# Optimization experiments

Hardware: AMD Instinct MI355X
Metric: run time of the kernel (lower is better)

The kernel has to match this reference:

```python
import jax, jax.numpy as jnp
import numpy as np

B, C, H, W = 8, 512, 64, 64
D = C // 8  # qk_downscale = 8


def setup_inputs() -> dict:
    key = jax.random.key(0)
    k1, k2, k3, k4, k5 = jax.random.split(key, 5)
    scale = 1.0 / np.sqrt(C)
    return {
        "x": jax.random.normal(k1, (B, C, H, W), dtype=jnp.float32),
        "Wq": jax.random.normal(k2, (D, C), dtype=jnp.float32) * scale,
        "Wk": jax.random.normal(k3, (D, C), dtype=jnp.float32) * scale,
        "Wv": jax.random.normal(k4, (C, C), dtype=jnp.float32) * scale,
        "gamma": jax.random.normal(k5, (1,), dtype=jnp.float32) * 0.1,
    }


def reference(x, Wq, Wk, Wv, gamma):
    b, c, h, w = x.shape
    n = h * w
    xf = x.reshape(b, c, n)                      # [B, C, N]
    # 1x1 Conv1d (bias=False) == channel matmul
    q = jnp.einsum('dc,bcn->bdn', Wq, xf)        # [B, D, N]
    k = jnp.einsum('dc,bcn->bdn', Wk, xf)        # [B, D, N]
    v = jnp.einsum('oc,bcn->bon', Wv, xf)        # [B, C, N]
    # torch.bmm(q.transpose(1,2), k) -> [B, N, N], unscaled
    qk = jnp.einsum('bdn,bdm->bnm', q, k)        # [B, N, N]
    # nn.Softmax(dim=1): normalize over the FIRST N axis (rows)
    attn = jax.nn.softmax(qk, axis=1)            # [B, N, N]
    # torch.bmm(v, qk_softmaxed) -> [B, C, N]
    out = gamma * jnp.einsum('bcn,bnm->bcm', v, attn) + xf
    return out.reshape(b, c, h, w)
```

## Files before the change

kernel.cpp:

```cpp
#include <hip/hip_runtime.h>
#include <math.h>
#include <stdint.h>

constexpr int Bn = 8;
constexpr int Cn = 512;
constexpr int Dn = 64;
constexpr int Nn = 4096;

typedef __bf16 bf16x8 __attribute__((ext_vector_type(8)));
typedef float  f32x16 __attribute__((ext_vector_type(16)));

typedef const __attribute__((address_space(1))) uint8_t* gptr_t;
typedef __attribute__((address_space(3))) uint8_t*       lptr_t;

static __device__ __forceinline__ uint32_t pkbf(float a, float b) {
    union { float f; uint32_t u; } x, y; x.f = a; y.f = b;
    uint32_t ra = (x.u + 0x7fffu + ((x.u >> 16) & 1u)) >> 16;
    uint32_t rb = (y.u + 0x7fffu + ((y.u >> 16) & 1u)) & 0xffff0000u;
    return ra | rb;
}

static __device__ __forceinline__ uint32_t cvt2(float a, float b) {
    union { __bf16 h[2]; uint32_t u; } p;
    p.h[0] = (__bf16)a; p.h[1] = (__bf16)b;
    return p.u;
}

static __device__ __forceinline__ float fexp2(float x) {
#if __has_builtin(__builtin_amdgcn_exp2f)
    return __builtin_amdgcn_exp2f(x);
#else
    return exp2f(x);
#endif
}

__global__ __launch_bounds__(256) void convert_w(
    const float* __restrict__ Wq, const float* __restrict__ Wk,
    const float* __restrict__ Wv, uint16_t* __restrict__ wb)
{
    int g = blockIdx.x * 256 + threadIdx.x;
    int tile = g >> 9;
    int s    = g & 511;
    int Ob = tile >> 3, cT = tile & 7;
    int ch = s >> 6,  o  = s & 63;
    const float* src;
    if (Ob == 0)       src = Wq + (size_t)o * Cn;
    else if (Ob == 1)  src = Wk + (size_t)o * Cn;
    else               src = Wv + (size_t)((Ob - 2) * 64 + o) * Cn;
    src += cT * 64 + ch * 8;
    float4 a = ((const float4*)src)[0];
    float4 c = ((const float4*)src)[1];
    uint4 u;
    u.x = pkbf(a.x, a.y); u.y = pkbf(a.z, a.w);
    u.z = pkbf(c.x, c.y); u.w = pkbf(c.z, c.w);
    *(uint4*)(wb + (size_t)g * 8) = u;
}

__global__ __launch_bounds__(256) void convert_x(
    const float* __restrict__ X, uint16_t* __restrict__ xt)
{
    __shared__ float Xs[64][68];
    const int ntile = blockIdx.x;
    const int cT    = blockIdx.y;
    const int b     = blockIdx.z;
    const int t  = threadIdx.x;
    const int lr = t >> 2;
    const int lc = (t & 3) << 4;
    const float* src = X + ((size_t)b * Cn + cT * 64 + lr) * Nn + ntile * 64 + lc;
    float4 v0 = ((const float4*)src)[0];
    float4 v1 = ((const float4*)src)[1];
    float4 v2 = ((const float4*)src)[2];
    float4 v3 = ((const float4*)src)[3];
    *(float4*)&Xs[lr][lc +  0] = v0;
    *(float4*)&Xs[lr][lc +  4] = v1;
    *(float4*)&Xs[lr][lc +  8] = v2;
    *(float4*)&Xs[lr][lc + 12] = v3;
    __syncthreads();
    const int nT = ntile >> 2, nb = ntile & 3;
    const size_t base = (((size_t)b * 16 + nT) * 8 + cT) * 8;
    #pragma unroll
    for (int ss = 0; ss < 2; ++ss) {
        int s  = t + ss * 256;
        int ch = s >> 6, nl = s & 63;
        uint4 u;
        u.x = pkbf(Xs[ch * 8 + 0][nl], Xs[ch * 8 + 1][nl]);
        u.y = pkbf(Xs[ch * 8 + 2][nl], Xs[ch * 8 + 3][nl]);
        u.z = pkbf(Xs[ch * 8 + 4][nl], Xs[ch * 8 + 5][nl]);
        u.w = pkbf(Xs[ch * 8 + 6][nl], Xs[ch * 8 + 7][nl]);
        *(uint4*)(xt + ((base + ch) * 256 + nb * 64 + nl) * 8) = u;
    }
}

__global__ __launch_bounds__(256, 2) void gemm_qkv(
    const uint16_t* __restrict__ wb, const uint16_t* __restrict__ xt,
    uint16_t* __restrict__ qt, uint16_t* __restrict__ kt,
    uint16_t* __restrict__ vt)
{
    __shared__ __align__(16) uint8_t Wlds[8192];
    __shared__ __align__(16) uint8_t Xlds[32768];
    const int nT = blockIdx.x;
    const int oB = blockIdx.y;
    const int b  = blockIdx.z;
    const int t    = threadIdx.x;
    const int lane = t & 63;
    const int wq   = __builtin_amdgcn_readfirstlane(t >> 6);
    const int mrow = lane & 31;
    const int qh   = lane >> 5;
    const uint8_t* wtiles = (const uint8_t*)wb + (size_t)oB * 8 * 8192;
    const uint8_t* xtiles = (const uint8_t*)xt + (((size_t)b * 16 + nT) * 8) * 32768;
    const bool isv = (oB >= 2);

    f32x16 acc[2][2];
    #pragma unroll
    for (int i = 0; i < 2; ++i)
        #pragma unroll
        for (int j = 0; j < 2; ++j)
            #pragma unroll
            for (int r = 0; r < 16; ++r) acc[i][j][r] = 0.f;

    for (int cT = 0; cT < 8; ++cT) {
        __syncthreads();
        #pragma unroll
        for (int i2 = 0; i2 < 2; ++i2) {
            int s = wq * 2 + i2;
            __builtin_amdgcn_global_load_lds(
                (gptr_t)(wtiles + cT * 8192 + s * 1024 + lane * 16),
                (lptr_t)(Wlds + s * 1024), 16, 0, 0);
        }
        #pragma unroll
        for (int i8 = 0; i8 < 8; ++i8) {
            int s = wq * 8 + i8;
            __builtin_amdgcn_global_load_lds(
                (gptr_t)(xtiles + cT * 32768 + s * 1024 + lane * 16),
                (lptr_t)(Xlds + s * 1024), 16, 0, 0);
        }
        __syncthreads();
        #pragma unroll
        for (int i = 0; i < 4; ++i) {
            int ch = 2 * i + qh;
            bf16x8 wf0 = *(const bf16x8*)(Wlds + ch * 1024 + mrow * 16);
            bf16x8 wf1 = *(const bf16x8*)(Wlds + ch * 1024 + (32 + mrow) * 16);
            bf16x8 xf0 = *(const bf16x8*)(Xlds + ch * 4096 + (wq * 64 + mrow) * 16);
            bf16x8 xf1 = *(const bf16x8*)(Xlds + ch * 4096 + (wq * 64 + 32 + mrow) * 16);
            if (!isv) {
                acc[0][0] = __builtin_amdgcn_mfma_f32_32x32x16_bf16(wf0, xf0, acc[0][0], 0, 0, 0);
                acc[0][1] = __builtin_amdgcn_mfma_f32_32x32x16_bf16(wf0, xf1, acc[0][1], 0, 0, 0);
                acc[1][0] = __builtin_amdgcn_mfma_f32_32x32x16_bf16(wf1, xf0, acc[1][0], 0, 0, 0);
                acc[1][1] = __builtin_amdgcn_mfma_f32_32x32x16_bf16(wf1, xf1, acc[1][1], 0, 0, 0);
            } else {
                acc[0][0] = __builtin_amdgcn_mfma_f32_32x32x16_bf16(xf0, wf0, acc[0][0], 0, 0, 0);
                acc[0][1] = __builtin_amdgcn_mfma_f32_32x32x16_bf16(xf0, wf1, acc[0][1], 0, 0, 0);
                acc[1][0] = __builtin_amdgcn_mfma_f32_32x32x16_bf16(xf1, wf0, acc[1][0], 0, 0, 0);
                acc[1][1] = __builtin_amdgcn_mfma_f32_32x32x16_bf16(xf1, wf1, acc[1][1], 0, 0, 0);
            }
        }
    }

    if (!isv) {
        uint16_t* dst = (oB == 0) ? qt : kt;
        const float qs = (oB == 0) ? 1.4426950408889634f : 1.0f;
        #pragma unroll
        for (int ot = 0; ot < 2; ++ot)
            #pragma unroll
            for (int ns = 0; ns < 2; ++ns) {
                int T = nT * 8 + wq * 2 + ns;
                size_t tb = ((size_t)b * 128 + T) * 2048;
                #pragma unroll
                for (int rr = 0; rr < 4; ++rr) {
                    uint2 u;
                    u.x = pkbf(qs * acc[ot][ns][4 * rr + 0], qs * acc[ot][ns][4 * rr + 1]);
                    u.y = pkbf(qs * acc[ot][ns][4 * rr + 2], qs * acc[ot][ns][4 * rr + 3]);
                    *(uint2*)(dst + tb + (size_t)(ot * 4 + rr) * 256 + mrow * 8 + 4 * qh) = u;
                }
            }
    } else {
        #pragma unroll
        for (int ns = 0; ns < 2; ++ns)
            #pragma unroll
            for (int ot = 0; ot < 2; ++ot) {
                int T = nT * 8 + wq * 2 + ns;
                int c_out = (oB - 2) * 64 + ot * 32 + mrow;
                size_t tb = ((size_t)b * 128 + T) * 16384;
                uint4 U0, U1;
                U0.x = pkbf(acc[ns][ot][ 0], acc[ns][ot][ 1]);
                U0.y = pkbf(acc[ns][ot][ 2], acc[ns][ot][ 3]);
                U0.z = pkbf(acc[ns][ot][ 4], acc[ns][ot][ 5]);
                U0.w = pkbf(acc[ns][ot][ 6], acc[ns][ot][ 7]);
                U1.x = pkbf(acc[ns][ot][ 8], acc[ns][ot][ 9]);
                U1.y = pkbf(acc[ns][ot][10], acc[ns][ot][11]);
                U1.z = pkbf(acc[ns][ot][12], acc[ns][ot][13]);
                U1.w = pkbf(acc[ns][ot][14], acc[ns][ot][15]);
                *(uint4*)(vt + tb + (size_t)qh      * 4096 + c_out * 8) = U0;
                *(uint4*)(vt + tb + (size_t)(2+qh)  * 4096 + c_out * 8) = U1;
            }
    }
}

__global__ __launch_bounds__(256, 2) void flash_attn(
    const uint16_t* __restrict__ qt, const uint16_t* __restrict__ kt,
    const uint16_t* __restrict__ vt, const float* __restrict__ X,
    const float* __restrict__ gamma, float* __restrict__ out)
{
    __shared__ __align__(16) uint8_t Klds[32768];
    __shared__ __align__(16) uint8_t Vlds[2][8192];

    const int bid = blockIdx.x;
    const int x   = bid & 7;
    const int kk  = bid >> 3;
    const int mB  = kk & 15;
    const int grp = (kk >> 4) * 8 + x;
    const int b   = grp >> 2;
    const int cB  = grp & 3;

    const int t    = threadIdx.x;
    const int lane = t & 63;
    const int wq   = __builtin_amdgcn_readfirstlane(t >> 6);
    const int mrow = lane & 31;
    const int qh   = lane >> 5;

    const uint8_t* kbase = (const uint8_t*)kt + ((size_t)b * 128 + (size_t)mB * 8) * 4096;
    const uint8_t* vbase = (const uint8_t*)vt + (size_t)b * 128 * 32768;
    const uint8_t* qbase = (const uint8_t*)qt + (size_t)b * 128 * 4096;

    #pragma unroll
    for (int i = 0; i < 8; ++i) {
        int s = wq * 8 + i;
        __builtin_amdgcn_global_load_lds((gptr_t)(kbase + s * 1024 + lane * 16),
                                         (lptr_t)(Klds + s * 1024), 16, 0, 0);
    }
    #pragma unroll
    for (int i = 0; i < 2; ++i) {
        __builtin_amdgcn_global_load_lds(
            (gptr_t)(vbase + wq * 8192 + cB * 2048 + i * 1024 + lane * 16),
            (lptr_t)(Vlds[0] + wq * 2048 + i * 1024), 16, 0, 0);
    }
    bf16x8 qnext[4];
    #pragma unroll
    for (int i = 0; i < 4; ++i)
        qnext[i] = *(const bf16x8*)(qbase + (2 * i + qh) * 512 + mrow * 16);
    __syncthreads();

    bf16x8 kfr[2][4];
    #pragma unroll
    for (int mt = 0; mt < 2; ++mt)
        #pragma unroll
        for (int i = 0; i < 4; ++i)
            kfr[mt][i] = *(const bf16x8*)(Klds + (wq * 2 + mt) * 4096
                                          + (2 * i + qh) * 512 + mrow * 16);

    f32x16 acc[2][4];
    #pragma unroll
    for (int mt = 0; mt < 2; ++mt)
        #pragma unroll
        for (int cf = 0; cf < 4; ++cf)
            #pragma unroll
            for (int r = 0; r < 16; ++r) acc[mt][cf][r] = 0.f;
    float lrun0 = 0.f, lrun1 = 0.f;

    constexpr float SBIAS = -86.5617024533378f;

    for (int T = 0; T < 128; ++T) {
        f32x16 S0, S1;
        #pragma unroll
        for (int r = 0; r < 16; ++r) { S0[r] = SBIAS; S1[r] = SBIAS; }
        #pragma unroll
        for (int i = 0; i < 4; ++i) {
            S0 = __builtin_amdgcn_mfma_f32_32x32x16_bf16(qnext[i], kfr[0][i], S0, 0, 0, 0);
            S1 = __builtin_amdgcn_mfma_f32_32x32x16_bf16(qnext[i], kfr[1][i], S1, 0, 0, 0);
        }

        if (T < 127) {
            const uint8_t* vsrc = vbase + (size_t)(T + 1) * 32768 + wq * 8192 + cB * 2048;
            uint8_t*       vdst = Vlds[(T + 1) & 1] + wq * 2048;
            #pragma unroll
            for (int i = 0; i < 2; ++i)
                __builtin_amdgcn_global_load_lds((gptr_t)(vsrc + i * 1024 + lane * 16),
                                                 (lptr_t)(vdst + i * 1024), 16, 0, 0);
            const uint8_t* qsrc = qbase + (size_t)(T + 1) * 4096;
            #pragma unroll
            for (int i = 0; i < 4; ++i)
                qnext[i] = *(const bf16x8*)(qsrc + (2 * i + qh) * 512 + mrow * 16);
        }

        union pu { uint32_t u[4]; bf16x8 v; };
        pu Pf[2][2];
        {
            float p[16], ps = 0.f;
            #pragma unroll
            for (int r = 0; r < 16; ++r) { p[r] = fexp2(S0[r]); ps += p[r]; }
            lrun0 += ps;
            #pragma unroll
            for (int j = 0; j < 4; ++j) Pf[0][0].u[j] = cvt2(p[2 * j],     p[2 * j + 1]);
            #pragma unroll
            for (int j = 0; j < 4; ++j) Pf[0][1].u[j] = cvt2(p[8 + 2 * j], p[8 + 2 * j + 1]);
        }
        {
            float p[16], ps = 0.f;
            #pragma unroll
            for (int r = 0; r < 16; ++r) { p[r] = fexp2(S1[r]); ps += p[r]; }
            lrun1 += ps;
            #pragma unroll
            for (int j = 0; j < 4; ++j) Pf[1][0].u[j] = cvt2(p[2 * j],     p[2 * j + 1]);
            #pragma unroll
            for (int j = 0; j < 4; ++j) Pf[1][1].u[j] = cvt2(p[8 + 2 * j], p[8 + 2 * j + 1]);
        }

        const uint8_t* vb_ = Vlds[T & 1];
        #pragma unroll
        for (int cf = 0; cf < 4; ++cf) {
            int cloc = cf * 32 + mrow;
            bf16x8 va = *(const bf16x8*)(vb_ + (size_t)qh       * 2048 + cloc * 16);
            bf16x8 vb = *(const bf16x8*)(vb_ + (size_t)(2 + qh) * 2048 + cloc * 16);
            #pragma unroll
            for (int mt = 0; mt < 2; ++mt) {
                acc[mt][cf] = __builtin_amdgcn_mfma_f32_32x32x16_bf16(va, Pf[mt][0].v, acc[mt][cf], 0, 0, 0);
                acc[mt][cf] = __builtin_amdgcn_mfma_f32_32x32x16_bf16(vb, Pf[mt][1].v, acc[mt][cf], 0, 0, 0);
            }
        }
        __syncthreads();
    }

    float Lm[2];
    Lm[0] = lrun0 + __shfl_xor(lrun0, 32);
    Lm[1] = lrun1 + __shfl_xor(lrun1, 32);
    const float g   = gamma[0];
    const float* xb = X   + (size_t)b * Cn * Nn;
    float*       ob = out + (size_t)b * Cn * Nn;
    #pragma unroll
    for (int mt = 0; mt < 2; ++mt) {
        const float scale = g / Lm[mt];
        const int   m     = mB * 256 + wq * 64 + mt * 32 + mrow;
        #pragma unroll
        for (int cf = 0; cf < 4; ++cf)
            #pragma unroll
            for (int r = 0; r < 16; ++r) {
                int c = cB * 128 + cf * 32 + (r & 3) + 8 * (r >> 2) + 4 * qh;
                size_t idx = (size_t)c * Nn + m;
                ob[idx] = scale * acc[mt][cf][r] + xb[idx];
            }
    }
}

extern "C" void kernel_launch(void* const* d_in, const int* in_sizes, int n_in,
                              void* d_out, int out_size, void* d_ws, size_t ws_size,
                              hipStream_t stream)
{
    const float* x     = (const float*)d_in[0];
    const float* Wq    = (const float*)d_in[1];
    const float* Wk    = (const float*)d_in[2];
    const float* Wv    = (const float*)d_in[3];
    const float* gamma = (const float*)d_in[4];
    float* out = (float*)d_out;

    uint16_t* qt = (uint16_t*)d_ws;
    uint16_t* kt = qt + (size_t)2097152;
    uint16_t* vt = kt + (size_t)2097152;
    uint16_t* xt = vt + (size_t)16777216;
    uint16_t* wbuf = xt + (size_t)16777216;

    convert_w <<<dim3(160),       256, 0, stream>>>(Wq, Wk, Wv, wbuf);
    convert_x <<<dim3(64, 8, 8),  256, 0, stream>>>(x, xt);
    gemm_qkv  <<<dim3(16, 10, 8), 256, 0, stream>>>(wbuf, xt, qt, kt, vt);
    flash_attn<<<dim3(512),       256, 0, stream>>>(qt, kt, vt, x, gamma, out);
}
```

Before: 368.6 us.

## Deepen V/Q prefetch to two tiles ahead via LDS with partial waitcnt barriers

Q tiles are now staged through LDS with global_load_lds instead of per-lane register loads. V and Q both use a 4-slot ring buffer that is prefetched two iterations ahead. The main loop is unrolled by two, and each full __syncthreads is replaced by a vmcnt(3) wait plus s_barrier, so one tile's loads stay in flight while the current tile is computed. This aims to hide global-load latency better, at the cost of more LDS (larger footprint may pressure the 2-blocks-per-CU occupancy) and extra LDS reads for Q.

```diff
diff --git a/kernel.cpp b/kernel.cpp
--- a/kernel.cpp
+++ b/kernel.cpp
@@ -202,7 +202,8 @@
     const float* __restrict__ gamma, float* __restrict__ out)
 {
     __shared__ __align__(16) uint8_t Klds[32768];
-    __shared__ __align__(16) uint8_t Vlds[2][8192];
+    __shared__ __align__(16) uint8_t Vlds[4][8192];
+    __shared__ __align__(16) uint8_t Qlds[4][4096];
 
     const int bid = blockIdx.x;
     const int x   = bid & 7;
@@ -229,15 +230,16 @@
                                          (lptr_t)(Klds + s * 1024), 16, 0, 0);
     }
     #pragma unroll
-    for (int i = 0; i < 2; ++i) {
+    for (int tt = 0; tt < 2; ++tt) {
+        #pragma unroll
+        for (int i = 0; i < 2; ++i)
+            __builtin_amdgcn_global_load_lds(
+                (gptr_t)(vbase + (size_t)tt * 32768 + wq * 8192 + cB * 2048 + i * 1024 + lane * 16),
+                (lptr_t)(Vlds[tt] + wq * 2048 + i * 1024), 16, 0, 0);
         __builtin_amdgcn_global_load_lds(
-            (gptr_t)(vbase + wq * 8192 + cB * 2048 + i * 1024 + lane * 16),
-            (lptr_t)(Vlds[0] + wq * 2048 + i * 1024), 16, 0, 0);
-    }
-    bf16x8 qnext[4];
-    #pragma unroll
-    for (int i = 0; i < 4; ++i)
-        qnext[i] = *(const bf16x8*)(qbase + (2 * i + qh) * 512 + mrow * 16);
+            (gptr_t)(qbase + (size_t)tt * 4096 + wq * 1024 + lane * 16),
+            (lptr_t)(Qlds[tt] + wq * 1024), 16, 0, 0);
+    }
     __syncthreads();
 
     bf16x8 kfr[2][4];
@@ -259,66 +261,95 @@
 
     constexpr float SBIAS = -86.5617024533378f;
 
-    for (int T = 0; T < 128; ++T) {
-        f32x16 S0, S1;
-        #pragma unroll
-        for (int r = 0; r < 16; ++r) { S0[r] = SBIAS; S1[r] = SBIAS; }
-        #pragma unroll
-        for (int i = 0; i < 4; ++i) {
-            S0 = __builtin_amdgcn_mfma_f32_32x32x16_bf16(qnext[i], kfr[0][i], S0, 0, 0, 0);
-            S1 = __builtin_amdgcn_mfma_f32_32x32x16_bf16(qnext[i], kfr[1][i], S1, 0, 0, 0);
-        }
-
-        if (T < 127) {
-            const uint8_t* vsrc = vbase + (size_t)(T + 1) * 32768 + wq * 8192 + cB * 2048;
-            uint8_t*       vdst = Vlds[(T + 1) & 1] + wq * 2048;
-            #pragma unroll
-            for (int i = 0; i < 2; ++i)
-                __builtin_amdgcn_global_load_lds((gptr_t)(vsrc + i * 1024 + lane * 16),
-                                                 (lptr_t)(vdst + i * 1024), 16, 0, 0);
-            const uint8_t* qsrc = qbase + (size_t)(T + 1) * 4096;
-            #pragma unroll
-            for (int i = 0; i < 4; ++i)
-                qnext[i] = *(const bf16x8*)(qsrc + (2 * i + qh) * 512 + mrow * 16);
-        }
-
-        union pu { uint32_t u[4]; bf16x8 v; };
-        pu Pf[2][2];
-        {
-            float p[16], ps = 0.f;
-            #pragma unroll
-            for (int r = 0; r < 16; ++r) { p[r] = fexp2(S0[r]); ps += p[r]; }
-            lrun0 += ps;
-            #pragma unroll
-            for (int j = 0; j < 4; ++j) Pf[0][0].u[j] = cvt2(p[2 * j],     p[2 * j + 1]);
-            #pragma unroll
-            for (int j = 0; j < 4; ++j) Pf[0][1].u[j] = cvt2(p[8 + 2 * j], p[8 + 2 * j + 1]);
-        }
-        {
-            float p[16], ps = 0.f;
-            #pragma unroll
-            for (int r = 0; r < 16; ++r) { p[r] = fexp2(S1[r]); ps += p[r]; }
-            lrun1 += ps;
-            #pragma unroll
-            for (int j = 0; j < 4; ++j) Pf[1][0].u[j] = cvt2(p[2 * j],     p[2 * j + 1]);
-            #pragma unroll
-            for (int j = 0; j < 4; ++j) Pf[1][1].u[j] = cvt2(p[8 + 2 * j], p[8 + 2 * j + 1]);
-        }
-
-        const uint8_t* vb_ = Vlds[T & 1];
-        #pragma unroll
-        for (int cf = 0; cf < 4; ++cf) {
-            int cloc = cf * 32 + mrow;
-            bf16x8 va = *(const bf16x8*)(vb_ + (size_t)qh       * 2048 + cloc * 16);
-            bf16x8 vb = *(const bf16x8*)(vb_ + (size_t)(2 + qh) * 2048 + cloc * 16);
-            #pragma unroll
-            for (int mt = 0; mt < 2; ++mt) {
-                acc[mt][cf] = __builtin_amdgcn_mfma_f32_32x32x16_bf16(va, Pf[mt][0].v, acc[mt][cf], 0, 0, 0);
-                acc[mt][cf] = __builtin_amdgcn_mfma_f32_32x32x16_bf16(vb, Pf[mt][1].v, acc[mt][cf], 0, 0, 0);
-            }
-        }
-        __syncthreads();
-    }
+#define FA_BODY(T_, STAGE_)                                                     \
+    do {                                                                        \
+        const int T__ = (T_);                                                   \
+          \
+                        \
+        if (STAGE_) {                                                           \
+            const int Tn__ = T__ + 2;                                           \
+            const uint8_t* vsrc__ = vbase + (size_t)Tn__ * 32768                \
+                                    + wq * 8192 + cB * 2048;                    \
+            uint8_t* vdst__ = Vlds[Tn__ & 3] + wq * 2048;                       \
+            __builtin_amdgcn_global_load_lds((gptr_t)(vsrc__ + lane * 16),      \
+                                             (lptr_t)(vdst__), 16, 0, 0);       \
+            __builtin_amdgcn_global_load_lds((gptr_t)(vsrc__ + 1024 + lane*16), \
+                                             (lptr_t)(vdst__ + 1024), 16, 0, 0);\
+            __builtin_amdgcn_global_load_lds(                                   \
+                (gptr_t)(qbase + (size_t)Tn__ * 4096 + wq * 1024 + lane * 16),  \
+                (lptr_t)(Qlds[Tn__ & 3] + wq * 1024), 16, 0, 0);                \
+        }                                                                       \
+                                                         \
+        const uint8_t* qb__ = Qlds[T__ & 3];                                    \
+        bf16x8 qf__[4];                                                         \
+        _Pragma("unroll")                                                       \
+        for (int i = 0; i < 4; ++i)                                             \
+            qf__[i] = *(const bf16x8*)(qb__ + (2 * i + qh) * 512 + mrow * 16);  \
+        f32x16 S0__, S1__;                                                      \
+        _Pragma("unroll")                                                       \
+        for (int r = 0; r < 16; ++r) { S0__[r] = SBIAS; S1__[r] = SBIAS; }      \
+        _Pragma("unroll")                                                       \
+        for (int i = 0; i < 4; ++i) {                                           \
+            S0__ = __builtin_amdgcn_mfma_f32_32x32x16_bf16(qf__[i], kfr[0][i], S0__, 0, 0, 0); \
+            S1__ = __builtin_amdgcn_mfma_f32_32x32x16_bf16(qf__[i], kfr[1][i], S1__, 0, 0, 0); \
+        }                                                                       \
+                      \
+        union pu__ { uint32_t u[4]; bf16x8 v; };                                \
+        pu__ Pf__[2][2];                                                        \
+        {                                                                       \
+            float p[16], ps = 0.f;                                              \
+            _Pragma("unroll")                                                   \
+            for (int r = 0; r < 16; ++r) { p[r] = fexp2(S0__[r]); ps += p[r]; } \
+            lrun0 += ps;                                                        \
+            _Pragma("unroll")                                                   \
+            for (int j = 0; j < 4; ++j) Pf__[0][0].u[j] = cvt2(p[2*j], p[2*j+1]); \
+            _Pragma("unroll")                                                   \
+            for (int j = 0; j < 4; ++j) Pf__[0][1].u[j] = cvt2(p[8+2*j], p[8+2*j+1]); \
+        }                                                                       \
+        {                                                                       \
+            float p[16], ps = 0.f;                                              \
+            _Pragma("unroll")                                                   \
+            for (int r = 0; r < 16; ++r) { p[r] = fexp2(S1__[r]); ps += p[r]; } \
+            lrun1 += ps;                                                        \
+            _Pragma("unroll")                                                   \
+            for (int j = 0; j < 4; ++j) Pf__[1][0].u[j] = cvt2(p[2*j], p[2*j+1]); \
+            _Pragma("unroll")                                                   \
+            for (int j = 0; j < 4; ++j) Pf__[1][1].u[j] = cvt2(p[8+2*j], p[8+2*j+1]); \
+        }                                                                       \
+                                                         \
+        const uint8_t* vb__ = Vlds[T__ & 3];                                    \
+        _Pragma("unroll")                                                       \
+        for (int cf = 0; cf < 4; ++cf) {                                        \
+            int cloc__ = cf * 32 + mrow;                                        \
+            bf16x8 va__ = *(const bf16x8*)(vb__ + (size_t)qh       * 2048 + cloc__ * 16); \
+            bf16x8 vc__ = *(const bf16x8*)(vb__ + (size_t)(2 + qh) * 2048 + cloc__ * 16); \
+            _Pragma("unroll")                                                   \
+            for (int mt = 0; mt < 2; ++mt) {                                    \
+                acc[mt][cf] = __builtin_amdgcn_mfma_f32_32x32x16_bf16(va__, Pf__[mt][0].v, acc[mt][cf], 0, 0, 0); \
+                acc[mt][cf] = __builtin_amdgcn_mfma_f32_32x32x16_bf16(vc__, Pf__[mt][1].v, acc[mt][cf], 0, 0, 0); \
+            }                                                                   \
+        }                                                                       \
+    } while (0)
+
+    for (int Tp = 0; Tp < 126; Tp += 2) {
+        FA_BODY(Tp, 1);
+        __builtin_amdgcn_sched_barrier(0);
+        asm volatile("s_waitcnt vmcnt(3)");
+        __builtin_amdgcn_s_barrier();
+        __builtin_amdgcn_sched_barrier(0);
+        FA_BODY(Tp + 1, 1);
+        __builtin_amdgcn_sched_barrier(0);
+        asm volatile("s_waitcnt vmcnt(3)");
+        __builtin_amdgcn_s_barrier();
+        __builtin_amdgcn_sched_barrier(0);
+    }
+    FA_BODY(126, 0);
+    __builtin_amdgcn_sched_barrier(0);
+    asm volatile("s_waitcnt vmcnt(0)");
+    __builtin_amdgcn_s_barrier();
+    __builtin_amdgcn_sched_barrier(0);
+    FA_BODY(127, 0);
+#undef FA_BODY
 
     float Lm[2];
     Lm[0] = lrun0 + __shfl_xor(lrun0, 32);
```

New measurement: 389.5 us. 5.7% more time.

## Drop LDS staging; load K and V fragments directly from global into registers

Applied to the files above, without the earlier changes.

Removes the shared-memory buffers for K and V. K fragments and per-iteration V fragments are now read straight from global memory into registers, and the per-iteration __syncthreads barrier is removed. Q for the next tile is prefetched into a separate register set and rotated at the end of each iteration. This avoids LDS round-trips and block-wide synchronisation, but each wave now issues its own global V loads with no cross-wave sharing and relies on cache hits, and register pressure rises.

```diff
diff --git a/kernel.cpp b/kernel.cpp
--- a/kernel.cpp
+++ b/kernel.cpp
@@ -201,9 +201,6 @@
     const uint16_t* __restrict__ vt, const float* __restrict__ X,
     const float* __restrict__ gamma, float* __restrict__ out)
 {
-    __shared__ __align__(16) uint8_t Klds[32768];
-    __shared__ __align__(16) uint8_t Vlds[2][8192];
-
     const int bid = blockIdx.x;
     const int x   = bid & 7;
     const int kk  = bid >> 3;
@@ -219,34 +216,22 @@
     const int qh   = lane >> 5;
 
     const uint8_t* kbase = (const uint8_t*)kt + ((size_t)b * 128 + (size_t)mB * 8) * 4096;
-    const uint8_t* vbase = (const uint8_t*)vt + (size_t)b * 128 * 32768;
+    const uint8_t* vbase = (const uint8_t*)vt + (size_t)b * 128 * 32768
+                           + (size_t)cB * 2048;
     const uint8_t* qbase = (const uint8_t*)qt + (size_t)b * 128 * 4096;
 
-    #pragma unroll
-    for (int i = 0; i < 8; ++i) {
-        int s = wq * 8 + i;
-        __builtin_amdgcn_global_load_lds((gptr_t)(kbase + s * 1024 + lane * 16),
-                                         (lptr_t)(Klds + s * 1024), 16, 0, 0);
-    }
-    #pragma unroll
-    for (int i = 0; i < 2; ++i) {
-        __builtin_amdgcn_global_load_lds(
-            (gptr_t)(vbase + wq * 8192 + cB * 2048 + i * 1024 + lane * 16),
-            (lptr_t)(Vlds[0] + wq * 2048 + i * 1024), 16, 0, 0);
-    }
-    bf16x8 qnext[4];
+    bf16x8 kfr[2][4];
+    #pragma unroll
+    for (int mt = 0; mt < 2; ++mt)
+        #pragma unroll
+        for (int i = 0; i < 4; ++i)
+            kfr[mt][i] = *(const bf16x8*)(kbase + (wq * 2 + mt) * 4096
+                                          + (2 * i + qh) * 512 + mrow * 16);
+
+    bf16x8 qcur[4];
     #pragma unroll
     for (int i = 0; i < 4; ++i)
-        qnext[i] = *(const bf16x8*)(qbase + (2 * i + qh) * 512 + mrow * 16);
-    __syncthreads();
-
-    bf16x8 kfr[2][4];
-    #pragma unroll
-    for (int mt = 0; mt < 2; ++mt)
-        #pragma unroll
-        for (int i = 0; i < 4; ++i)
-            kfr[mt][i] = *(const bf16x8*)(Klds + (wq * 2 + mt) * 4096
-                                          + (2 * i + qh) * 512 + mrow * 16);
+        qcur[i] = *(const bf16x8*)(qbase + (2 * i + qh) * 512 + mrow * 16);
 
     f32x16 acc[2][4];
     #pragma unroll
@@ -260,26 +245,29 @@
     constexpr float SBIAS = -86.5617024533378f;
 
     for (int T = 0; T < 128; ++T) {
-        f32x16 S0, S1;
-        #pragma unroll
-        for (int r = 0; r < 16; ++r) { S0[r] = SBIAS; S1[r] = SBIAS; }
-        #pragma unroll
-        for (int i = 0; i < 4; ++i) {
-            S0 = __builtin_amdgcn_mfma_f32_32x32x16_bf16(qnext[i], kfr[0][i], S0, 0, 0, 0);
-            S1 = __builtin_amdgcn_mfma_f32_32x32x16_bf16(qnext[i], kfr[1][i], S1, 0, 0, 0);
-        }
-
+        const uint8_t* vb_ = vbase + (size_t)T * 32768;
+        bf16x8 vfA[4], vfC[4];
+        #pragma unroll
+        for (int cf = 0; cf < 4; ++cf) {
+            int cloc = cf * 32 + mrow;
+            vfA[cf] = *(const bf16x8*)(vb_ + (size_t)qh       * 8192 + cloc * 16);
+            vfC[cf] = *(const bf16x8*)(vb_ + (size_t)(2 + qh) * 8192 + cloc * 16);
+        }
+        bf16x8 qnext[4];
         if (T < 127) {
-            const uint8_t* vsrc = vbase + (size_t)(T + 1) * 32768 + wq * 8192 + cB * 2048;
-            uint8_t*       vdst = Vlds[(T + 1) & 1] + wq * 2048;
-            #pragma unroll
-            for (int i = 0; i < 2; ++i)
-                __builtin_amdgcn_global_load_lds((gptr_t)(vsrc + i * 1024 + lane * 16),
-                                                 (lptr_t)(vdst + i * 1024), 16, 0, 0);
             const uint8_t* qsrc = qbase + (size_t)(T + 1) * 4096;
             #pragma unroll
             for (int i = 0; i < 4; ++i)
                 qnext[i] = *(const bf16x8*)(qsrc + (2 * i + qh) * 512 + mrow * 16);
+        }
+
+        f32x16 S0, S1;
+        #pragma unroll
+        for (int r = 0; r < 16; ++r) { S0[r] = SBIAS; S1[r] = SBIAS; }
+        #pragma unroll
+        for (int i = 0; i < 4; ++i) {
+            S0 = __builtin_amdgcn_mfma_f32_32x32x16_bf16(qcur[i], kfr[0][i], S0, 0, 0, 0);
+            S1 = __builtin_amdgcn_mfma_f32_32x32x16_bf16(qcur[i], kfr[1][i], S1, 0, 0, 0);
         }
 
         union pu { uint32_t u[4]; bf16x8 v; };
@@ -305,19 +293,17 @@
             for (int j = 0; j < 4; ++j) Pf[1][1].u[j] = cvt2(p[8 + 2 * j], p[8 + 2 * j + 1]);
         }
 
-        const uint8_t* vb_ = Vlds[T & 1];
         #pragma unroll
         for (int cf = 0; cf < 4; ++cf) {
-            int cloc = cf * 32 + mrow;
-            bf16x8 va = *(const bf16x8*)(vb_ + (size_t)qh       * 2048 + cloc * 16);
-            bf16x8 vb = *(const bf16x8*)(vb_ + (size_t)(2 + qh) * 2048 + cloc * 16);
             #pragma unroll
             for (int mt = 0; mt < 2; ++mt) {
-                acc[mt][cf] = __builtin_amdgcn_mfma_f32_32x32x16_bf16(va, Pf[mt][0].v, acc[mt][cf], 0, 0, 0);
-                acc[mt][cf] = __builtin_amdgcn_mfma_f32_32x32x16_bf16(vb, Pf[mt][1].v, acc[mt][cf], 0, 0, 0);
-            }
-        }
-        __syncthreads();
+                acc[mt][cf] = __builtin_amdgcn_mfma_f32_32x32x16_bf16(vfA[cf], Pf[mt][0].v, acc[mt][cf], 0, 0, 0);
+                acc[mt][cf] = __builtin_amdgcn_mfma_f32_32x32x16_bf16(vfC[cf], Pf[mt][1].v, acc[mt][cf], 0, 0, 0);
+            }
+        }
+
+        #pragma unroll
+        for (int i = 0; i < 4; ++i) qcur[i] = qnext[i];
     }
 
     float Lm[2];
```

Result: no change. 366.4 us (-0.6%).
